# Optimization experiments

Measured on AMD Instinct MI355X. Metric: run time of the kernel, lower is better.

## Reference

```python
import jax, jax.numpy as jnp
import numpy as np

N_MEL = 80; H = 512; HD = H // 2; R = 2; A = 128; NF = 32; K = 31
EMB = 512; ENC = 512; NSYM = 100


def _lstm_layer(x, lengths, Wih, Whh, b):
    # x: [B,T,D]; masked unidirectional LSTM (packed-sequence semantics:
    # state frozen and output zero past each sequence length).
    B, T, _ = x.shape
    Hh = Whh.shape[1]
    def step(carry, inp):
        h, c = carry
        xt, t = inp
        g = xt @ Wih.T + h @ Whh.T + b
        i, f, gg, o = jnp.split(g, 4, axis=-1)
        c_new = jax.nn.sigmoid(f) * c + jax.nn.sigmoid(i) * jnp.tanh(gg)
        h_new = jax.nn.sigmoid(o) * jnp.tanh(c_new)
        m = (t < lengths)[:, None]
        return (jnp.where(m, h_new, h), jnp.where(m, c_new, c)), jnp.where(m, h_new, 0.0)
    init = (jnp.zeros((B, Hh), x.dtype), jnp.zeros((B, Hh), x.dtype))
    _, ys = jax.lax.scan(step, init, (x.transpose(1, 0, 2), jnp.arange(T)))
    return ys.transpose(1, 0, 2)


def _bilstm(x, lengths, fw, bw):
    # bidirectional masked LSTM: backward dir runs on the sequence reversed
    # within its valid length (pack_padded_sequence semantics).
    T = x.shape[1]
    t = jnp.arange(T)
    idx = jnp.clip(lengths[:, None] - 1 - t[None, :], 0)
    x_rev = jnp.take_along_axis(x, idx[:, :, None], axis=1)
    out_f = _lstm_layer(x, lengths, *fw)
    out_r = _lstm_layer(x_rev, lengths, *bw)
    out_b = jnp.take_along_axis(out_r, idx[:, :, None], axis=1)
    out_b = jnp.where((t[None, :] < lengths[:, None])[:, :, None], out_b, 0.0)
    return jnp.concatenate([out_f, out_b], axis=-1)


def _forward(mel, mel_lengths, decoder_inputs, start_embedding,
             l1f_Wih, l1f_Whh, l1f_b, l1b_Wih, l1b_Whh, l1b_b,
             l2f_Wih, l2f_Whh, l2f_b, l2b_Wih, l2b_Whh, l2b_b,
             dec_Wih, dec_Whh, dec_b,
             q_W, m_W, loc_conv_W, loc_W, v_W,
             ph_W, ph_b, ps_W, ps_b):
    B = mel.shape[0]
    x = mel.transpose(0, 2, 1)                                   # [B,T,80]
    out1 = _bilstm(x, mel_lengths, (l1f_Wih, l1f_Whh, l1f_b), (l1b_Wih, l1b_Whh, l1b_b))
    out1 = out1.reshape(B, -1, H * R)                             # [B,T/R,H*R]
    mem_len = jnp.ceil(mel_lengths.astype(jnp.float32) / R).astype(jnp.int32)
    memory = _bilstm(out1, mem_len, (l2f_Wih, l2f_Whh, l2f_b), (l2b_Wih, l2b_Whh, l2b_b))  # [B,T',H]
    Tm = memory.shape[1]
    pad_mask = jnp.arange(Tm)[None, :] >= mem_len[:, None]        # True where padded
    processed_memory = memory @ m_W.T                             # [B,T',A]

    dec_seq = jnp.concatenate([start_embedding[None], decoder_inputs.transpose(2, 0, 1)], axis=0)  # [T+1,B,EMB]

    pad = (K - 1) // 2

    def dec_step(state, dinp):
        h, c, aw, awc, ctx = state
        cell_in = jnp.concatenate([dinp, ctx], axis=-1)
        g = cell_in @ dec_Wih.T + h @ dec_Whh.T + dec_b
        i, f, gg, o = jnp.split(g, 4, axis=-1)
        c = jax.nn.sigmoid(f) * c + jax.nn.sigmoid(i) * jnp.tanh(gg)
        h = jax.nn.sigmoid(o) * jnp.tanh(c)
        # location-sensitive attention
        aw_cat = jnp.stack([aw, awc], axis=1)                     # [B,2,T']
        loc = jax.lax.conv_general_dilated(aw_cat, loc_conv_W, (1,), [(pad, pad)],
                                           dimension_numbers=('NCH', 'OIH', 'NCH'))
        loc = loc.transpose(0, 2, 1) @ loc_W.T                    # [B,T',A]
        q = (h @ q_W.T)[:, None, :]                               # [B,1,A]
        e = jnp.tanh(q + loc + processed_memory) @ v_W.T          # [B,T',1]
        e = jnp.where(pad_mask, -1e9, e[..., 0])
        aw_new = jax.nn.softmax(e, axis=1)
        ctx_new = jnp.einsum('bt,btd->bd', aw_new, memory)
        awc_new = awc + aw_new
        hid = jax.nn.relu(jnp.concatenate([h, ctx_new], axis=-1) @ ph_W.T + ph_b)
        logit = hid @ ps_W.T + ps_b                               # dropout is identity in eval
        return (h, c, aw_new, awc_new, ctx_new), (hid, logit, aw_new)

    z = jnp.zeros((B, H), mel.dtype)
    init = (z, z, jnp.zeros((B, Tm), mel.dtype), jnp.zeros((B, Tm), mel.dtype), z)
    _, (hiddens, logits, aligns) = jax.lax.scan(dec_step, init, dec_seq)
    return (hiddens.transpose(1, 0, 2), logits.transpose(1, 0, 2), aligns.transpose(1, 0, 2))


def setup_inputs() -> dict:
    key = jax.random.key(0)
    ks = iter(jax.random.split(key, 40))
    B, T, TD = 32, 1600, 160
    s = 0.05
    def w(shape):
        return jax.random.normal(next(ks), shape, jnp.float32) * s
    mel_lengths = jax.random.randint(next(ks), (B,), T // 2, T + 1)
    mel_lengths = mel_lengths.at[0].set(T)
    return {
        'mel': jax.random.normal(next(ks), (B, N_MEL, T), jnp.float32),
        'mel_lengths': mel_lengths,
        'decoder_inputs': jax.random.normal(next(ks), (B, EMB, TD), jnp.float32),
        'start_embedding': jax.random.normal(next(ks), (B, EMB), jnp.float32),
        'l1f_Wih': w((4 * HD, N_MEL)), 'l1f_Whh': w((4 * HD, HD)), 'l1f_b': w((4 * HD,)),
        'l1b_Wih': w((4 * HD, N_MEL)), 'l1b_Whh': w((4 * HD, HD)), 'l1b_b': w((4 * HD,)),
        'l2f_Wih': w((4 * HD, H * R)), 'l2f_Whh': w((4 * HD, HD)), 'l2f_b': w((4 * HD,)),
        'l2b_Wih': w((4 * HD, H * R)), 'l2b_Whh': w((4 * HD, HD)), 'l2b_b': w((4 * HD,)),
        'dec_Wih': w((4 * H, EMB + H)), 'dec_Whh': w((4 * H, H)), 'dec_b': w((4 * H,)),
        'q_W': w((A, H)), 'm_W': w((A, H)), 'loc_conv_W': w((NF, 2, K)),
        'loc_W': w((A, NF)), 'v_W': w((1, A)),
        'ph_W': w((ENC, H + H)), 'ph_b': w((ENC,)),
        'ps_W': w((NSYM + 1, ENC)), 'ps_b': w((NSYM + 1,)),
    }


def reference(mel, mel_lengths, decoder_inputs, start_embedding,
              l1f_Wih, l1f_Whh, l1f_b, l1b_Wih, l1b_Whh, l1b_b,
              l2f_Wih, l2f_Whh, l2f_b, l2b_Wih, l2b_Whh, l2b_b,
              dec_Wih, dec_Whh, dec_b,
              q_W, m_W, loc_conv_W, loc_W, v_W,
              ph_W, ph_b, ps_W, ps_b):
    return _forward(mel, mel_lengths, decoder_inputs, start_embedding,
                    l1f_Wih, l1f_Whh, l1f_b, l1b_Wih, l1b_Whh, l1b_b,
                    l2f_Wih, l2f_Whh, l2f_b, l2b_Wih, l2b_Whh, l2b_b,
                    dec_Wih, dec_Whh, dec_b,
                    q_W, m_W, loc_conv_W, loc_W, v_W,
                    ph_W, ph_b, ps_W, ps_b)
```

## Files before the change

kernel.cpp:

```cpp
#include <hip/hip_runtime.h>
#include <hip/hip_bf16.h>

typedef __hip_bfloat16 bf16;
typedef __attribute__((ext_vector_type(8))) short short8v;
typedef __attribute__((ext_vector_type(4))) float float4v;
#define DEVINL __device__ __forceinline__

DEVINL float bfu2f(unsigned int u){ union{unsigned int u; float f;} c; c.u=u; return c.f; }
DEVINL float b2f(bf16 v){ return __bfloat162float(v); }
DEVINL bf16  f2b(float f){ return __float2bfloat16(f); }
DEVINL float sigf(float x){ return 1.f/(1.f+__expf(-x)); }
DEVINL float tanhfast(float x){
  float t=__expf(-2.f*fabsf(x));
  float r=(1.f-t)/(1.f+t);
  return copysignf(r,x);
}
DEVINL void hilo(float x, short& h, short& l){
  bf16 hb = __float2bfloat16(x);
  bf16 lb = __float2bfloat16(x - __bfloat162float(hb));
  h = *(short*)&hb; l = *(short*)&lb;
}
DEVINL void ld4(const bf16* __restrict__ p, float* d){
  uint2 v = *reinterpret_cast<const uint2*>(p);
  d[0]=bfu2f(v.x<<16); d[1]=bfu2f(v.x&0xffff0000u);
  d[2]=bfu2f(v.y<<16); d[3]=bfu2f(v.y&0xffff0000u);
}
DEVINL void ld4(const float* __restrict__ p, float* d){
  float4 v = *reinterpret_cast<const float4*>(p);
  d[0]=v.x; d[1]=v.y; d[2]=v.z; d[3]=v.w;
}
DEVINL void st1(bf16* p, float v){ *p = f2b(v); }
DEVINL void st1(float* p, float v){ *p = v; }

__global__ void k_zero_f(float* p, long n){
  long i=(long)blockIdx.x*256+threadIdx.x, st=(long)gridDim.x*256;
  for(;i<n;i+=st) p[i]=0.f;
}
__global__ void k_zero_b(bf16* p, long n){
  long i=(long)blockIdx.x*256+threadIdx.x, st=(long)gridDim.x*256;
  for(;i<n;i+=st) p[i]=f2b(0.f);
}
__global__ void k_xT96b(const float* __restrict__ mel, bf16* __restrict__ xT){
  int i = blockIdx.x*256+threadIdx.x; if(i>=51200*96) return;
  int m = i/96, d = i - m*96; int b = m/1600, t = m - b*1600;
  xT[i] = f2b((d<80)? mel[((size_t)b*80 + d)*1600 + t] : 0.f);
}
__global__ void k_padW96b2(const float* __restrict__ W, bf16* __restrict__ hi,
                           bf16* __restrict__ lo){
  int i = blockIdx.x*256+threadIdx.x; if(i>=1024*96) return;
  int j=i/96, d=i-j*96;
  float x = (d<80)? W[j*80+d] : 0.f;
  short h,l; hilo(x,h,l);
  hi[i]=*(bf16*)&h; lo[i]=*(bf16*)&l;
}
__global__ void k_cvt2(const float* __restrict__ W, bf16* __restrict__ hi,
                       bf16* __restrict__ lo, int n){
  int i=blockIdx.x*256+threadIdx.x; if(i>=n) return;
  short h,l; hilo(W[i], h, l);
  hi[i]=*(bf16*)&h; lo[i]=*(bf16*)&l;
}
__global__ void k_whh_il8(const float* __restrict__ W, bf16* __restrict__ il){
  int i = blockIdx.x*256+threadIdx.x; if(i>=262144) return;
  int kk = i&7; int j = (i>>3)&1023; int kc = i>>13;
  il[i] = f2b(W[j*256 + kc*8 + kk]);
}
__global__ void k_psW(const float* __restrict__ W, const float* __restrict__ bsrc,
                      float* __restrict__ Wp, float* __restrict__ bp){
  int i=blockIdx.x*256+threadIdx.x;
  if(i<128*512){ int n=i/512,k=i-n*512; Wp[i] = (n<101)? W[n*512+k] : 0.f; }
  else if(i<128*512+128){ int n=i-128*512; bp[n]=(n<101)? bsrc[n]:0.f; }
}
__global__ void k_dseqb(const float* __restrict__ start, const float* __restrict__ dec_in,
                        bf16* __restrict__ dseq){
  int i=blockIdx.x*256+threadIdx.x; if(i>=5152*512) return;
  int r=i/512, e=i-r*512; int s=r/32, b=r-s*32;
  dseq[i] = f2b((s==0)? start[b*512+e] : dec_in[(size_t)b*81920 + e*160 + (s-1)]);
}
__global__ void k_wpd(const float* __restrict__ Wih, bf16* __restrict__ hi,
                      bf16* __restrict__ lo){
  int i=blockIdx.x*256+threadIdx.x; if(i>=2048*512) return;
  int j=i>>9, k=i&511;
  short h,l; hilo(Wih[(size_t)j*1024 + k], h, l);
  hi[i]=*(bf16*)&h; lo[i]=*(bf16*)&l;
}

template<bool RELU, typename TA, typename TCO>
__global__ __launch_bounds__(256) void gemm64(
    const TA* __restrict__ A, int lda, int T, int TC, int t0,
    const int* __restrict__ lens, int lenDiv, int rev,
    const float* __restrict__ W, int ldw,
    const float* __restrict__ bias,
    TCO* __restrict__ C, int ldc, int K)
{
  __shared__ float As[16][64];
  __shared__ float Ws[16][64];
  const int tid = threadIdx.x;
  const int n0 = blockIdx.x*64, m0 = blockIdx.y*64;
  const int tx = tid & 15, ty = tid >> 4;
  const int r = tid >> 2, c4 = (tid & 3) * 4;
  const int m = m0 + r;
  size_t arow;
  if (lens){
    int b = m / TC, tc = m - b*TC, t = t0 + tc;
    if (rev){
      int L = lens[b]; if (lenDiv==2) L=(L+1)>>1;
      t = L-1-t; if (t<0) t=0;
    }
    arow = (size_t)b*T + t;
  } else arow = (size_t)m;
  float acc[4][4] = {{0.f}};
  for (int k0=0; k0<K; k0+=16){
    float av[4];
    ld4(A + arow*lda + k0 + c4, av);
    const float4 wv = *reinterpret_cast<const float4*>(&W[(size_t)(n0+r)*ldw + k0 + c4]);
    As[c4+0][r] = av[0]; As[c4+1][r] = av[1]; As[c4+2][r] = av[2]; As[c4+3][r] = av[3];
    Ws[c4+0][r] = wv.x; Ws[c4+1][r]=wv.y; Ws[c4+2][r]=wv.z; Ws[c4+3][r]=wv.w;
    __syncthreads();
    #pragma unroll
    for(int k=0;k<16;k++){
      const float4 a = *reinterpret_cast<const float4*>(&As[k][ty*4]);
      const float4 w = *reinterpret_cast<const float4*>(&Ws[k][tx*4]);
      acc[0][0] += a.x*w.x; acc[0][1] += a.x*w.y; acc[0][2] += a.x*w.z; acc[0][3] += a.x*w.w;
      acc[1][0] += a.y*w.x; acc[1][1] += a.y*w.y; acc[1][2] += a.y*w.z; acc[1][3] += a.y*w.w;
      acc[2][0] += a.z*w.x; acc[2][1] += a.z*w.y; acc[2][2] += a.z*w.z; acc[2][3] += a.z*w.w;
      acc[3][0] += a.w*w.x; acc[3][1] += a.w*w.y; acc[3][2] += a.w*w.z; acc[3][3] += a.w*w.w;
    }
    __syncthreads();
  }
  #pragma unroll
  for(int i=0;i<4;i++){
    const size_t row = (size_t)m0 + ty*4 + i;
    #pragma unroll
    for(int j=0;j<4;j++){
      const int col = n0 + tx*4 + j;
      float v = acc[i][j] + (bias ? bias[col] : 0.f);
      if (RELU) v = fmaxf(v, 0.f);
      st1(&C[row*ldc + col], v);
    }
  }
}

template<bool RELU, typename TCO>
__global__ __launch_bounds__(256) void gemmM(
    const bf16* __restrict__ A, int lda, int T, int TC, int t0,
    const int* __restrict__ lens, int lenDiv, int rev,
    const short* __restrict__ Whi, const short* __restrict__ Wlo, int ldw,
    const float* __restrict__ bias,
    TCO* __restrict__ C, int ldc, int K)
{
  __shared__ short As[128][40];
  __shared__ short Bs[2][128][40];
  const int tid = threadIdx.x;
  const int lane = tid & 63, wave = tid >> 6;
  const int wm = wave >> 1, wn = wave & 1;
  const int n0 = blockIdx.x*128, m0 = blockIdx.y*128;

  auto arow_of = [&](int m)->size_t{
    if (lens){
      int b = m / TC, tc = m - b*TC, t = t0 + tc;
      if (rev){ int L=lens[b]; if(lenDiv==2) L=(L+1)>>1; t=L-1-t; if(t<0)t=0; }
      return (size_t)b*T + t;
    }
    return (size_t)m;
  };

  float4v acc[4][4];
  #pragma unroll
  for (int i=0;i<4;++i)
    #pragma unroll
    for (int j=0;j<4;++j) acc[i][j] = (float4v){0.f,0.f,0.f,0.f};

  const int ar = tid>>2, akp = (tid&3)*8;
  const size_t arow0 = arow_of(m0 + ar), arow1 = arow_of(m0 + ar + 64);
  const short* Ash = (const short*)A;

  for (int k0=0; k0<K; k0+=32){
    *(short8v*)&As[ar][akp]    = *(const short8v*)(Ash + arow0*lda + k0 + akp);
    *(short8v*)&As[ar+64][akp] = *(const short8v*)(Ash + arow1*lda + k0 + akp);
    *(short8v*)&Bs[0][ar][akp]    = *(const short8v*)(Whi + (size_t)(n0+ar)*ldw + k0 + akp);
    *(short8v*)&Bs[0][ar+64][akp] = *(const short8v*)(Whi + (size_t)(n0+ar+64)*ldw + k0 + akp);
    *(short8v*)&Bs[1][ar][akp]    = *(const short8v*)(Wlo + (size_t)(n0+ar)*ldw + k0 + akp);
    *(short8v*)&Bs[1][ar+64][akp] = *(const short8v*)(Wlo + (size_t)(n0+ar+64)*ldw + k0 + akp);
    __syncthreads();
    const int l15 = lane & 15, kb8 = (lane>>4)*8;
    short8v a0[4], bh[4], bl[4];
    #pragma unroll
    for (int mt=0;mt<4;++mt) a0[mt] = *(const short8v*)&As[wm*64+mt*16+l15][kb8];
    #pragma unroll
    for (int nt=0;nt<4;++nt){
      bh[nt] = *(const short8v*)&Bs[0][wn*64+nt*16+l15][kb8];
      bl[nt] = *(const short8v*)&Bs[1][wn*64+nt*16+l15][kb8];
    }
    #pragma unroll
    for (int mt=0;mt<4;++mt)
      #pragma unroll
      for (int nt=0;nt<4;++nt){
        acc[mt][nt] = __builtin_amdgcn_mfma_f32_16x16x32_bf16(a0[mt], bh[nt], acc[mt][nt], 0,0,0);
        acc[mt][nt] = __builtin_amdgcn_mfma_f32_16x16x32_bf16(a0[mt], bl[nt], acc[mt][nt], 0,0,0);
      }
    __syncthreads();
  }
  const int l15 = lane & 15, rb = (lane>>4)*4;
  #pragma unroll
  for (int mt=0;mt<4;++mt){
    #pragma unroll
    for (int nt=0;nt<4;++nt){
      const int col = n0 + wn*64 + nt*16 + l15;
      const float bv = bias ? bias[col] : 0.f;
      #pragma unroll
      for (int i=0;i<4;++i){
        const size_t row = (size_t)m0 + wm*64 + mt*16 + rb + i;
        float v = acc[mt][nt][i] + bv;
        if (RELU) v = fmaxf(v, 0.f);
        st1(&C[row*ldc + col], v);
      }
    }
  }
}

__global__ __launch_bounds__(1024) void lstm8(
   const bf16* __restrict__ Pf, const bf16* __restrict__ Pb,
   const bf16* __restrict__ Whf, const bf16* __restrict__ Whb,
   const int* __restrict__ lens, int lenDiv, int t0, int TC,
   bf16* __restrict__ out, int T, float* __restrict__ hc)
{
  const int b = blockIdx.x, dir = blockIdx.y, j = threadIdx.x;
  int L = lens[b]; if (lenDiv==2) L = (L+1)>>1;
  const bf16* P  = (dir ? Pb : Pf) + (size_t)b*TC*1024;
  const bf16* wil = (dir ? Whb : Whf) + (size_t)j*8;
  float* hcp = hc + (size_t)(dir*32+b)*512;
  __shared__ float hs[256];
  __shared__ float gs[1024];
  if (j<256) hs[j] = hcp[j];
  float c = (j<256) ? hcp[256+j] : 0.f;
  __syncthreads();
  int tcEnd = L - t0; if (tcEnd > TC) tcEnd = TC;
  for (int tc=0; tc<tcEnd; ++tc){
    float acc = b2f(P[(size_t)tc*1024 + j]);
    #pragma unroll 8
    for (int kc=0; kc<32; ++kc){
      const uint4 wv = *reinterpret_cast<const uint4*>(wil + (size_t)kc*8192);
      const int k = kc*8;
      acc += bfu2f(wv.x<<16)*hs[k]   + bfu2f(wv.x&0xffff0000u)*hs[k+1]
           + bfu2f(wv.y<<16)*hs[k+2] + bfu2f(wv.y&0xffff0000u)*hs[k+3]
           + bfu2f(wv.z<<16)*hs[k+4] + bfu2f(wv.z&0xffff0000u)*hs[k+5]
           + bfu2f(wv.w<<16)*hs[k+6] + bfu2f(wv.w&0xffff0000u)*hs[k+7];
    }
    gs[j] = acc;
    __syncthreads();
    if (j<256){
      const float cn = sigf(gs[256+j])*c + sigf(gs[j])*tanhfast(gs[512+j]);
      const float hn = sigf(gs[768+j])*tanhfast(cn);
      c = cn;
      const int t = t0+tc;
      const int srow = dir ? (L-1-t) : t;
      out[((size_t)b*T + srow)*512 + dir*256 + j] = f2b(hn);
      hs[j] = hn;
    }
    __syncthreads();
  }
  if (j<256){ hcp[j]=hs[j]; hcp[256+j]=c; }
}

__global__ __launch_bounds__(256) void dec_g(
  const bf16* __restrict__ Pd, const float* __restrict__ Wih,
  const float* __restrict__ Whh, const float* __restrict__ h_state,
  const float* __restrict__ ctx_state, float* __restrict__ g_buf, int s)
{
  const int b = blockIdx.x, jt = blockIdx.y, tid = threadIdx.x;
  const int j = jt*256 + tid;
  __shared__ float cs[512], hs[512];
  cs[tid] = ctx_state[b*512+tid]; cs[256+tid] = ctx_state[b*512+256+tid];
  hs[tid] = h_state[b*512+tid];   hs[256+tid] = h_state[b*512+256+tid];
  __syncthreads();
  float acc = b2f(Pd[((size_t)(s*32+b))*2048 + j]);
  const float* wc = Wih + (size_t)j*1024 + 512;
  const float* wh = Whh + (size_t)j*512;
  for (int k=0;k<512;k+=4){
    const float4 cv = *(const float4*)&cs[k];
    const float4 hv = *(const float4*)&hs[k];
    const float4 a  = *(const float4*)&wc[k];
    const float4 b4 = *(const float4*)&wh[k];
    acc += a.x*cv.x + a.y*cv.y + a.z*cv.z + a.w*cv.w;
    acc += b4.x*hv.x + b4.y*hv.y + b4.z*hv.z + b4.w*hv.w;
  }
  g_buf[b*2048 + j] = acc;
}

__global__ __launch_bounds__(1024) void dec_rest(
  const float* __restrict__ g_buf, const float* __restrict__ qW,
  const float* __restrict__ convW, const float* __restrict__ locW,
  const float* __restrict__ vW, const float* __restrict__ PM, const bf16* __restrict__ memB,
  const int* __restrict__ lens,
  float* __restrict__ h_state, float* __restrict__ c_state, float* __restrict__ ctx_state,
  float* __restrict__ aw_state, float* __restrict__ awc_state,
  float* __restrict__ hallctx, float* __restrict__ outA, int s)
{
  const int b = blockIdx.x, u = threadIdx.x;
  __shared__ float hsh[512], red[1024], aw_s[800], q_s[128], v_s[128];
  __shared__ float convW_s[1984], locW_s[4096];
  for (int i=u; i<1984; i+=1024) convW_s[i]=convW[i];
  for (int i=u; i<4096; i+=1024) locW_s[i]=locW[i];
  if (u<128) v_s[u]=vW[u];
  if (u<512){
    const float gi = g_buf[b*2048 + u],     gf = g_buf[b*2048+512+u];
    const float gg = g_buf[b*2048+1024+u],  go = g_buf[b*2048+1536+u];
    const float cn = sigf(gf)*c_state[b*512+u] + sigf(gi)*tanhfast(gg);
    const float hn = sigf(go)*tanhfast(cn);
    c_state[b*512+u]=cn; h_state[b*512+u]=hn; hsh[u]=hn;
    hallctx[((size_t)(s*32+b))*1024 + u] = hn;
  }
  __syncthreads();
  if (u<128){
    const float* wr = qW + u*512;
    float acc=0.f;
    for (int k=0;k<512;k+=4){
      const float4 w = *(const float4*)&wr[k];
      const float4 h = *(const float4*)&hsh[k];
      acc += w.x*h.x + w.y*h.y + w.z*h.z + w.w*h.w;
    }
    q_s[u]=acc;
  }
  __syncthreads();
  const int mlen = (lens[b]+1)>>1;
  const int t = u;
  float ex = 0.f;
  if (t < 800 && t < mlen){
    float convf[32];
    #pragma unroll
    for (int f=0;f<32;++f) convf[f]=0.f;
    for (int k=0;k<31;++k){
      const int pos = t-15+k;
      const bool ok = (pos>=0 && pos<800);
      const float a0 = ok ? aw_state[b*800+pos] : 0.f;
      const float a1 = ok ? awc_state[b*800+pos] : 0.f;
      #pragma unroll
      for (int f=0;f<32;++f)
        convf[f] += convW_s[(f*2+0)*31+k]*a0 + convW_s[(f*2+1)*31+k]*a1;
    }
    const float* pm = PM + ((size_t)b*800 + t)*128;
    float e = 0.f;
    for (int a=0;a<128;++a){
      float loc = 0.f;
      #pragma unroll
      for (int f=0;f<32;++f) loc += convf[f]*locW_s[a*32+f];
      e += v_s[a]*tanhfast(q_s[a]+loc+pm[a]);
    }
    ex = __expf(e);
  }
  red[u]=ex; __syncthreads();
  for (int st=512; st>0; st>>=1){
    if (u<st) red[u]+=red[u+st];
    __syncthreads();
  }
  const float invZ = 1.f/red[0];
  if (t<800){
    const float a0 = ex*invZ;
    aw_s[t]=a0; aw_state[b*800+t]=a0; awc_state[b*800+t]+=a0;
    outA[((size_t)b*161+s)*800+t] = a0;
  }
  __syncthreads();
  {
    const int half = u>>9, d = u&511;
    float acc=0.f;
    const int tb = half*400;
    for (int t2=tb; t2<tb+400; ++t2)
      acc += aw_s[t2]*b2f(memB[((size_t)b*800+t2)*512 + d]);
    red[half*512 + d] = acc;
  }
  __syncthreads();
  if (u<512){
    const float v = red[u] + red[512+u];
    ctx_state[b*512+u]=v;
    hallctx[((size_t)(s*32+b))*1024 + 512 + u] = v;
  }
}

__global__ void k_scat_h(const float* __restrict__ hid, float* __restrict__ outH){
  int i=blockIdx.x*256+threadIdx.x; if(i>=5152*512) return;
  int r=i>>9, d=i&511; int s=r>>5, b=r&31;
  outH[((size_t)b*161+s)*512 + d] = hid[i];
}
__global__ void k_scat_l(const float* __restrict__ lg, float* __restrict__ outL){
  int i=blockIdx.x*256+threadIdx.x; if(i>=5152*101) return;
  int r=i/101, n=i-r*101; int s=r>>5, b=r&31;
  outL[((size_t)b*161+s)*101 + n] = lg[r*128+n];
}

extern "C" void kernel_launch(void* const* d_in, const int* in_sizes, int n_in,
                              void* d_out, int out_size, void* d_ws, size_t ws_size,
                              hipStream_t stream)
{
  const float* mel    = (const float*)d_in[0];
  const int*   lens   = (const int*)  d_in[1];
  const float* dec_in = (const float*)d_in[2];
  const float* start  = (const float*)d_in[3];
  const float* l1fWih = (const float*)d_in[4];
  const float* l1fWhh = (const float*)d_in[5];
  const float* l1fb   = (const float*)d_in[6];
  const float* l1bWih = (const float*)d_in[7];
  const float* l1bWhh = (const float*)d_in[8];
  const float* l1bb   = (const float*)d_in[9];
  const float* l2fWih = (const float*)d_in[10];
  const float* l2fWhh = (const float*)d_in[11];
  const float* l2fb   = (const float*)d_in[12];
  const float* l2bWih = (const float*)d_in[13];
  const float* l2bWhh = (const float*)d_in[14];
  const float* l2bb   = (const float*)d_in[15];
  const float* decWih = (const float*)d_in[16];
  const float* decWhh = (const float*)d_in[17];
  const float* decb   = (const float*)d_in[18];
  const float* qW     = (const float*)d_in[19];
  const float* mW     = (const float*)d_in[20];
  const float* convW  = (const float*)d_in[21];
  const float* locW   = (const float*)d_in[22];
  const float* vW     = (const float*)d_in[23];
  const float* phW    = (const float*)d_in[24];
  const float* phb    = (const float*)d_in[25];
  const float* psW    = (const float*)d_in[26];
  const float* psb    = (const float*)d_in[27];
  (void)in_sizes; (void)n_in; (void)out_size; (void)ws_size;

  char* wsp = (char*)d_ws;
  size_t off = 0;
  auto alloc = [&](size_t bytes)->char*{
    char* p = wsp + off; off += (bytes + 255) & ~(size_t)255; return p;
  };

  float* stateF   = (float*)alloc((size_t)100352*4);
  float* h_state  = stateF;
  float* c_state  = stateF + 16384;
  float* ctx_state= stateF + 32768;
  float* aw_state = stateF + 49152;
  float* awc_state= stateF + 74752;
  float* hc_enc   = (float*)alloc((size_t)32768*4);
  float* g_buf    = (float*)alloc((size_t)65536*4);
  float* psW_p    = (float*)alloc((size_t)65536*4);
  float* psb_p    = (float*)alloc((size_t)128*4);
  bf16*  whh1f    = (bf16*)alloc((size_t)262144*2);
  bf16*  whh1b    = (bf16*)alloc((size_t)262144*2);
  bf16*  whh2f    = (bf16*)alloc((size_t)262144*2);
  bf16*  whh2b    = (bf16*)alloc((size_t)262144*2);
  bf16*  w_m_h    = (bf16*)alloc((size_t)65536*2);
  bf16*  w_m_l    = (bf16*)alloc((size_t)65536*2);
  bf16*  w_l1f_h  = (bf16*)alloc((size_t)98304*2);
  bf16*  w_l1f_l  = (bf16*)alloc((size_t)98304*2);
  bf16*  w_l1b_h  = (bf16*)alloc((size_t)98304*2);
  bf16*  w_l1b_l  = (bf16*)alloc((size_t)98304*2);

  char* R_X = alloc((size_t)10747904);
  bf16*  xTb   = (bf16*)R_X;
  bf16*  w_l2f_h = (bf16*)R_X;
  bf16*  w_l2f_l = (bf16*)(R_X + 2097152);
  bf16*  w_l2b_h = (bf16*)(R_X + 4194304);
  bf16*  w_l2b_l = (bf16*)(R_X + 6291456);
  bf16*  dseqB = (bf16*)R_X;
  bf16*  w_pd_h = (bf16*)(R_X + 5505024);
  bf16*  w_pd_l = (bf16*)(R_X + 7602176);
  float* hid  = (float*)R_X;
  char* R_P = alloc((size_t)26214400);
  bf16* Pchf = (bf16*)R_P;
  bf16* Pchb = (bf16*)(R_P + 10485760);
  bf16* Pd   = (bf16*)R_P;
  float* logitb = (float*)(R_P + 21495808);
  char* R_O = alloc((size_t)52428800);
  bf16*  out1    = (bf16*)R_O;
  float* PM      = (float*)R_O;
  float* hallctx = (float*)(R_O + 13107200);
  char* R_M = alloc((size_t)26214400);
  bf16*  memB = (bf16*)R_M;

  float* outF = (float*)d_out;
  float* outH = outF;
  float* outL = outF + 2637824;
  float* outA = outF + 3158176;

  k_zero_f<<<392,256,0,stream>>>(stateF, 100352);
  k_zero_f<<<128,256,0,stream>>>(hc_enc, 32768);
  k_xT96b<<<19200,256,0,stream>>>(mel, xTb);
  k_padW96b2<<<384,256,0,stream>>>(l1fWih, w_l1f_h, w_l1f_l);
  k_padW96b2<<<384,256,0,stream>>>(l1bWih, w_l1b_h, w_l1b_l);
  k_whh_il8<<<1024,256,0,stream>>>(l1fWhh, whh1f);
  k_whh_il8<<<1024,256,0,stream>>>(l1bWhh, whh1b);
  k_whh_il8<<<1024,256,0,stream>>>(l2fWhh, whh2f);
  k_whh_il8<<<1024,256,0,stream>>>(l2bWhh, whh2b);
  k_cvt2<<<256,256,0,stream>>>(mW, w_m_h, w_m_l, 65536);
  k_psW<<<257,256,0,stream>>>(psW, psb, psW_p, psb_p);
  k_zero_b<<<2048,256,0,stream>>>(out1, 26214400);
  k_zero_b<<<2048,256,0,stream>>>(memB, 13107200);

  for (int c=0;c<10;++c){
    const int t0 = c*160;
    gemmM<false,bf16><<<dim3(8,40),256,0,stream>>>(xTb,96, 1600,160,t0, lens,1,0,
        (const short*)w_l1f_h,(const short*)w_l1f_l,96, l1fb, Pchf,1024, 96);
    gemmM<false,bf16><<<dim3(8,40),256,0,stream>>>(xTb,96, 1600,160,t0, lens,1,1,
        (const short*)w_l1b_h,(const short*)w_l1b_l,96, l1bb, Pchb,1024, 96);
    lstm8<<<dim3(32,2),1024,0,stream>>>(Pchf,Pchb, whh1f,whh1b, lens,1, t0,160, out1, 1600, hc_enc);
  }

  k_cvt2<<<4096,256,0,stream>>>(l2fWih, w_l2f_h, w_l2f_l, 1048576);
  k_cvt2<<<4096,256,0,stream>>>(l2bWih, w_l2b_h, w_l2b_l, 1048576);

  k_zero_f<<<128,256,0,stream>>>(hc_enc, 32768);
  for (int c=0;c<5;++c){
    const int t0 = c*160;
    gemmM<false,bf16><<<dim3(8,40),256,0,stream>>>(out1,1024, 800,160,t0, lens,2,0,
        (const short*)w_l2f_h,(const short*)w_l2f_l,1024, l2fb, Pchf,1024, 1024);
    gemmM<false,bf16><<<dim3(8,40),256,0,stream>>>(out1,1024, 800,160,t0, lens,2,1,
        (const short*)w_l2b_h,(const short*)w_l2b_l,1024, l2bb, Pchb,1024, 1024);
    lstm8<<<dim3(32,2),1024,0,stream>>>(Pchf,Pchb, whh2f,whh2b, lens,2, t0,160, memB, 800, hc_enc);
  }

  gemmM<false,float><<<dim3(1,200),256,0,stream>>>(memB,512, 0,0,0, nullptr,0,0,
      (const short*)w_m_h,(const short*)w_m_l,512, (const float*)nullptr, PM,128, 512);
  k_zero_b<<<2048,256,0,stream>>>(dseqB, 2686976);
  k_dseqb<<<10304,256,0,stream>>>(start, dec_in, dseqB);
  k_wpd<<<4096,256,0,stream>>>(decWih, w_pd_h, w_pd_l);
  gemmM<false,bf16><<<dim3(16,41),256,0,stream>>>(dseqB,512, 0,0,0, nullptr,0,0,
      (const short*)w_pd_h,(const short*)w_pd_l,512, decb, Pd,2048, 512);
  k_zero_f<<<2048,256,0,stream>>>(hallctx, 5308416);

  for (int s=0; s<161; ++s){
    dec_g<<<dim3(32,8),256,0,stream>>>(Pd, decWih, decWhh, h_state, ctx_state, g_buf, s);
    dec_rest<<<32,1024,0,stream>>>(g_buf, qW, convW, locW, vW, PM, memB, lens,
                                   h_state, c_state, ctx_state, aw_state, awc_state,
                                   hallctx, outA, s);
  }

  gemm64<true ,float,float><<<dim3(8,81),256,0,stream>>>(hallctx,1024, 0,0,0, nullptr,0,0,
                                                phW,1024, phb, hid,512, 1024);
  gemm64<false,float,float><<<dim3(2,81),256,0,stream>>>(hid,512, 0,0,0, nullptr,0,0,
                                                psW_p,512, psb_p, logitb,128, 512);
  k_scat_h<<<10304,256,0,stream>>>(hid, outH);
  k_scat_l<<<2033,256,0,stream>>>(logitb, outL);
}
```

Measured before the change: 37.95 ms.

## Split LSTM recurrence across four blocks with LDS-resident weights and atomic barrier

Replaces the one-block-per-sequence LSTM recurrence kernel with four cooperating 512-thread blocks per sequence and direction. Each block keeps its 64-column slice of the recurrent weight matrix resident in LDS, with a rotated layout, instead of re-reading all of W_hh from cache every timestep. Per-step partial gate sums go to a double-buffered global buffer, and the four blocks synchronise through an atomic arrival counter. This trades repeated weight streaming for a cross-block spin barrier every step. That barrier relies on all 256 blocks being resident at the same time, and it adds global atomic latency to each step.

After: 39.56 ms. 1.04x slower.

```diff
diff --git a/kernel.cpp b/kernel.cpp
--- a/kernel.cpp
+++ b/kernel.cpp
@@ -53,16 +53,14 @@
   short h,l; hilo(x,h,l);
   hi[i]=*(bf16*)&h; lo[i]=*(bf16*)&l;
 }
+__global__ void k_cvt(const float* __restrict__ W, bf16* __restrict__ o, int n){
+  int i=blockIdx.x*256+threadIdx.x; if(i<n) o[i]=f2b(W[i]);
+}
 __global__ void k_cvt2(const float* __restrict__ W, bf16* __restrict__ hi,
                        bf16* __restrict__ lo, int n){
   int i=blockIdx.x*256+threadIdx.x; if(i>=n) return;
   short h,l; hilo(W[i], h, l);
   hi[i]=*(bf16*)&h; lo[i]=*(bf16*)&l;
-}
-__global__ void k_whh_il8(const float* __restrict__ W, bf16* __restrict__ il){
-  int i = blockIdx.x*256+threadIdx.x; if(i>=262144) return;
-  int kk = i&7; int j = (i>>3)&1023; int kc = i>>13;
-  il[i] = f2b(W[j*256 + kc*8 + kk]);
 }
 __global__ void k_psW(const float* __restrict__ W, const float* __restrict__ bsrc,
                       float* __restrict__ Wp, float* __restrict__ bp){
@@ -218,48 +216,89 @@
   }
 }
 
-__global__ __launch_bounds__(1024) void lstm8(
+__global__ __launch_bounds__(512) void lstm16(
    const bf16* __restrict__ Pf, const bf16* __restrict__ Pb,
    const bf16* __restrict__ Whf, const bf16* __restrict__ Whb,
    const int* __restrict__ lens, int lenDiv, int t0, int TC,
-   bf16* __restrict__ out, int T, float* __restrict__ hc)
+   bf16* __restrict__ out, int T, float* __restrict__ hc,
+   float* __restrict__ part, int* __restrict__ arrive)
 {
-  const int b = blockIdx.x, dir = blockIdx.y, j = threadIdx.x;
+  const int q = blockIdx.x, b = blockIdx.y, dir = blockIdx.z;
+  const int tid = threadIdx.x;
+  const int g = dir*32 + b;
   int L = lens[b]; if (lenDiv==2) L = (L+1)>>1;
-  const bf16* P  = (dir ? Pb : Pf) + (size_t)b*TC*1024;
-  const bf16* wil = (dir ? Whb : Whf) + (size_t)j*8;
-  float* hcp = hc + (size_t)(dir*32+b)*512;
-  __shared__ float hs[256];
-  __shared__ float gs[1024];
-  if (j<256) hs[j] = hcp[j];
-  float c = (j<256) ? hcp[256+j] : 0.f;
+  int tcEnd = L - t0; if (tcEnd > TC) tcEnd = TC;
+  const bf16* P = (dir ? Pb : Pf) + (size_t)b*TC*1024;
+  const short* Wg = (const short*)(dir ? Whb : Whf);
+  float* hcp = hc + (size_t)g*512;
+  float* partg = part + (size_t)g*8192;
+  int* arr = arrive + g;
+
+  __shared__ short wl[65536];
+  __shared__ float hq[64];
+
+  for (int pass=0; pass<16; ++pass){
+    const int r = pass*64 + (tid>>3);
+    const int li = tid & 7;
+    const uint4 v = *(const uint4*)(Wg + (size_t)r*256 + q*64 + li*8);
+    const int kk0 = li*2;
+    *(uint2*)&wl[r*64 + (((kk0  ) + r)&15)*4] = make_uint2(v.x, v.y);
+    *(uint2*)&wl[r*64 + (((kk0+1) + r)&15)*4] = make_uint2(v.z, v.w);
+  }
+  if (tid < 64) hq[tid] = hcp[q*64 + tid];
+  float c = (tid < 64) ? hcp[256 + q*64 + tid] : 0.f;
   __syncthreads();
-  int tcEnd = L - t0; if (tcEnd > TC) tcEnd = TC;
+
+  int par = 0;
   for (int tc=0; tc<tcEnd; ++tc){
-    float acc = b2f(P[(size_t)tc*1024 + j]);
-    #pragma unroll 8
-    for (int kc=0; kc<32; ++kc){
-      const uint4 wv = *reinterpret_cast<const uint4*>(wil + (size_t)kc*8192);
-      const int k = kc*8;
-      acc += bfu2f(wv.x<<16)*hs[k]   + bfu2f(wv.x&0xffff0000u)*hs[k+1]
-           + bfu2f(wv.y<<16)*hs[k+2] + bfu2f(wv.y&0xffff0000u)*hs[k+3]
-           + bfu2f(wv.z<<16)*hs[k+4] + bfu2f(wv.z&0xffff0000u)*hs[k+5]
-           + bfu2f(wv.w<<16)*hs[k+6] + bfu2f(wv.w&0xffff0000u)*hs[k+7];
-    }
-    gs[j] = acc;
-    __syncthreads();
-    if (j<256){
-      const float cn = sigf(gs[256+j])*c + sigf(gs[j])*tanhfast(gs[512+j]);
-      const float hn = sigf(gs[768+j])*tanhfast(cn);
+    const int r0 = tid, r1 = 512 + tid;
+    float a0 = 0.f, a1 = 0.f;
+    #pragma unroll
+    for (int kk=0; kk<16; ++kk){
+      const float4 h4 = *(const float4*)&hq[kk*4];
+      const uint2 w0 = *(const uint2*)&wl[r0*64 + ((kk + r0)&15)*4];
+      const uint2 w1 = *(const uint2*)&wl[r1*64 + ((kk + r1)&15)*4];
+      a0 += bfu2f(w0.x<<16)*h4.x + bfu2f(w0.x&0xffff0000u)*h4.y
+          + bfu2f(w0.y<<16)*h4.z + bfu2f(w0.y&0xffff0000u)*h4.w;
+      a1 += bfu2f(w1.x<<16)*h4.x + bfu2f(w1.x&0xffff0000u)*h4.y
+          + bfu2f(w1.y<<16)*h4.z + bfu2f(w1.y&0xffff0000u)*h4.w;
+    }
+    par = tc & 1;
+    atomicExch(&partg[par*4096 + q*1024 + r0], a0);
+    atomicExch(&partg[par*4096 + q*1024 + r1], a1);
+    __syncthreads();
+    if (tid == 0){
+      atomicAdd(arr, 1);
+      const int target = 4*(tc+1);
+      while (atomicAdd(arr, 0) < target) __builtin_amdgcn_s_sleep(2);
+    }
+    __syncthreads();
+    if (tid < 64){
+      const int unit = q*64 + tid;
+      float gv[4];
+      #pragma unroll
+      for (int gi=0; gi<4; ++gi){
+        const int row = gi*256 + unit;
+        float s = b2f(P[(size_t)tc*1024 + row]);
+        #pragma unroll
+        for (int qq=0; qq<4; ++qq)
+          s += atomicAdd(&partg[par*4096 + qq*1024 + row], 0.f);
+        gv[gi] = s;
+      }
+      const float cn = sigf(gv[1])*c + sigf(gv[0])*tanhfast(gv[2]);
+      const float hn = sigf(gv[3])*tanhfast(cn);
       c = cn;
-      const int t = t0+tc;
+      const int t = t0 + tc;
       const int srow = dir ? (L-1-t) : t;
-      out[((size_t)b*T + srow)*512 + dir*256 + j] = f2b(hn);
-      hs[j] = hn;
-    }
-    __syncthreads();
-  }
-  if (j<256){ hcp[j]=hs[j]; hcp[256+j]=c; }
+      out[((size_t)b*T + srow)*512 + dir*256 + unit] = f2b(hn);
+      hq[tid] = hn;
+    }
+    __syncthreads();
+  }
+  if (tcEnd > 0 && tid < 64){
+    hcp[q*64 + tid] = hq[tid];
+    hcp[256 + q*64 + tid] = c;
+  }
 }
 
 __global__ __launch_bounds__(256) void dec_g(
@@ -437,6 +476,8 @@
   float* g_buf    = (float*)alloc((size_t)65536*4);
   float* psW_p    = (float*)alloc((size_t)65536*4);
   float* psb_p    = (float*)alloc((size_t)128*4);
+  float* part     = (float*)alloc((size_t)524288*4);
+  int*   arrive   = (int*)  alloc((size_t)64*4);
   bf16*  whh1f    = (bf16*)alloc((size_t)262144*2);
   bf16*  whh1b    = (bf16*)alloc((size_t)262144*2);
   bf16*  whh2f    = (bf16*)alloc((size_t)262144*2);
@@ -480,10 +521,10 @@
   k_xT96b<<<19200,256,0,stream>>>(mel, xTb);
   k_padW96b2<<<384,256,0,stream>>>(l1fWih, w_l1f_h, w_l1f_l);
   k_padW96b2<<<384,256,0,stream>>>(l1bWih, w_l1b_h, w_l1b_l);
-  k_whh_il8<<<1024,256,0,stream>>>(l1fWhh, whh1f);
-  k_whh_il8<<<1024,256,0,stream>>>(l1bWhh, whh1b);
-  k_whh_il8<<<1024,256,0,stream>>>(l2fWhh, whh2f);
-  k_whh_il8<<<1024,256,0,stream>>>(l2bWhh, whh2b);
+  k_cvt<<<1024,256,0,stream>>>(l1fWhh, whh1f, 262144);
+  k_cvt<<<1024,256,0,stream>>>(l1bWhh, whh1b, 262144);
+  k_cvt<<<1024,256,0,stream>>>(l2fWhh, whh2f, 262144);
+  k_cvt<<<1024,256,0,stream>>>(l2bWhh, whh2b, 262144);
   k_cvt2<<<256,256,0,stream>>>(mW, w_m_h, w_m_l, 65536);
   k_psW<<<257,256,0,stream>>>(psW, psb, psW_p, psb_p);
   k_zero_b<<<2048,256,0,stream>>>(out1, 26214400);
@@ -495,7 +536,9 @@
         (const short*)w_l1f_h,(const short*)w_l1f_l,96, l1fb, Pchf,1024, 96);
     gemmM<false,bf16><<<dim3(8,40),256,0,stream>>>(xTb,96, 1600,160,t0, lens,1,1,
         (const short*)w_l1b_h,(const short*)w_l1b_l,96, l1bb, Pchb,1024, 96);
-    lstm8<<<dim3(32,2),1024,0,stream>>>(Pchf,Pchb, whh1f,whh1b, lens,1, t0,160, out1, 1600, hc_enc);
+    k_zero_f<<<1,64,0,stream>>>((float*)arrive, 64);
+    lstm16<<<dim3(4,32,2),512,0,stream>>>(Pchf,Pchb, whh1f,whh1b, lens,1, t0,160,
+                                          out1, 1600, hc_enc, part, arrive);
   }
 
   k_cvt2<<<4096,256,0,stream>>>(l2fWih, w_l2f_h, w_l2f_l, 1048576);
@@ -508,7 +551,9 @@
         (const short*)w_l2f_h,(const short*)w_l2f_l,1024, l2fb, Pchf,1024, 1024);
     gemmM<false,bf16><<<dim3(8,40),256,0,stream>>>(out1,1024, 800,160,t0, lens,2,1,
         (const short*)w_l2b_h,(const short*)w_l2b_l,1024, l2bb, Pchb,1024, 1024);
-    lstm8<<<dim3(32,2),1024,0,stream>>>(Pchf,Pchb, whh2f,whh2b, lens,2, t0,160, memB, 800, hc_enc);
+    k_zero_f<<<1,64,0,stream>>>((float*)arrive, 64);
+    lstm16<<<dim3(4,32,2),512,0,stream>>>(Pchf,Pchb, whh2f,whh2b, lens,2, t0,160,
+                                          memB, 800, hc_enc, part, arrive);
   }
 
   gemmM<false,float><<<dim3(1,200),256,0,stream>>>(memB,512, 0,0,0, nullptr,0,0,
```
